# Performance work log

Hardware: AMD Instinct MI355X
Metric: run time of the kernel (lower is better)

## Reference

```python
import jax, jax.numpy as jnp
import numpy as np

DIM = 4096
N_HEADS = 32
N_KV_HEADS = 8
HEAD_DIM = DIM // N_HEADS
N_REP = N_HEADS // N_KV_HEADS
SEQ_LEN = 2048
ROPE_THETA = 10000.0


def rope_cos_sin(head_dim, seq_len, theta):
    freqs = 1.0 / (theta ** (jnp.arange(0, head_dim, 2, dtype=jnp.float32) / head_dim))  # [hd/2]
    t = jnp.arange(seq_len, dtype=jnp.float32)
    angles = jnp.outer(t, freqs)  # [S, hd/2]
    return jnp.cos(angles), jnp.sin(angles)


def apply_rope(x, cos, sin):
    # x: [B, S, H, hd]; complex rotation on interleaved (even, odd) pairs
    xr = x[..., 0::2].astype(jnp.float32)
    xi = x[..., 1::2].astype(jnp.float32)
    c = cos[None, :, None, :]
    s = sin[None, :, None, :]
    out_r = xr * c - xi * s
    out_i = xr * s + xi * c
    out = jnp.stack([out_r, out_i], axis=-1).reshape(x.shape)
    return out.astype(x.dtype)


def setup_inputs() -> dict:
    key = jax.random.key(0)
    ks = jax.random.split(key, 5)
    x = jax.random.normal(ks[0], (1, SEQ_LEN, DIM), dtype=jnp.float32)
    wq = jax.random.normal(ks[1], (DIM, DIM), dtype=jnp.float32) * (DIM ** -0.5)
    wk = jax.random.normal(ks[2], (N_KV_HEADS * HEAD_DIM, DIM), dtype=jnp.float32) * (DIM ** -0.5)
    wv = jax.random.normal(ks[3], (N_KV_HEADS * HEAD_DIM, DIM), dtype=jnp.float32) * (DIM ** -0.5)
    wo = jax.random.normal(ks[4], (DIM, DIM), dtype=jnp.float32) * (DIM ** -0.5)
    return {"x": x, "start_pos": 0, "wq": wq, "wk": wk, "wv": wv, "wo": wo}


def reference(x, start_pos, wq, wk, wv, wo):
    bsz, seq_len, _ = x.shape
    # projections (torch Linear: y = x @ W.T)
    xq = (x @ wq.T).reshape(bsz, seq_len, N_HEADS, HEAD_DIM)
    xk = (x @ wk.T).reshape(bsz, seq_len, N_KV_HEADS, HEAD_DIM)
    xv = (x @ wv.T).reshape(bsz, seq_len, N_KV_HEADS, HEAD_DIM)

    cos, sin = rope_cos_sin(HEAD_DIM, seq_len, ROPE_THETA)
    xq = apply_rope(xq, cos, sin)
    xk = apply_rope(xk, cos, sin)

    # repeat_kv (GQA): [B, S, Hkv, hd] -> [B, S, Hkv*n_rep, hd]
    keys = jnp.repeat(xk, N_REP, axis=2)
    values = jnp.repeat(xv, N_REP, axis=2)

    # [B, H, S, hd]
    q = xq.transpose(0, 2, 1, 3)
    k = keys.transpose(0, 2, 1, 3)
    v = values.transpose(0, 2, 1, 3)

    scale = 1.0 / jnp.sqrt(jnp.asarray(HEAD_DIM, dtype=jnp.float32))
    scores = jnp.einsum('bhqd,bhkd->bhqk', q, k) * scale  # [B, H, S, S]
    causal = jnp.tril(jnp.ones((seq_len, seq_len), dtype=bool))
    scores = jnp.where(causal[None, None], scores, -jnp.inf)
    attn = jax.nn.softmax(scores.astype(jnp.float32), axis=-1).astype(q.dtype)
    out = jnp.einsum('bhqk,bhkd->bhqd', attn, v)  # [B, H, S, hd]
    out = out.transpose(0, 2, 1, 3).reshape(bsz, seq_len, -1)
    return out @ wo.T
```

## Files before the change

kernel.cpp:

```cpp
#include <hip/hip_runtime.h>

#define DIM 4096
#define KVDIM 1024
#define KVSTRIDE 2048
#define SEQ 2048
#define HEADS 32
#define HD 128

typedef __attribute__((ext_vector_type(8))) short bf16x8;
typedef __attribute__((ext_vector_type(4))) float f32x4;

__device__ inline unsigned short f2bf(float f) {
    union { float f; unsigned int u; } v; v.f = f;
    unsigned int r = v.u + 0x7fffu + ((v.u >> 16) & 1u);
    return (unsigned short)(r >> 16);
}
__device__ inline float bf2f(unsigned short h) {
    union { unsigned int u; float f; } v; v.u = ((unsigned int)h) << 16;
    return v.f;
}

__device__ inline void gld16(const void* g, void* l) {
    __builtin_amdgcn_global_load_lds(
        (const __attribute__((address_space(1))) void*)g,
        (__attribute__((address_space(3))) void*)l, 16, 0, 0);
}

__global__ void convert_f32_bf16(const float* __restrict__ in,
                                 unsigned short* __restrict__ out, int n) {
    int i = (blockIdx.x * blockDim.x + threadIdx.x) * 8;
    if (i >= n) return;
    const float4* p = (const float4*)(in + i);
    float4 a = p[0], b = p[1];
    bf16x8 o;
    o[0] = (short)f2bf(a.x); o[1] = (short)f2bf(a.y);
    o[2] = (short)f2bf(a.z); o[3] = (short)f2bf(a.w);
    o[4] = (short)f2bf(b.x); o[5] = (short)f2bf(b.y);
    o[6] = (short)f2bf(b.z); o[7] = (short)f2bf(b.w);
    *(bf16x8*)(out + i) = o;
}

__global__ void rope_table(float* __restrict__ cs, float* __restrict__ sn) {
    int i = blockIdx.x * blockDim.x + threadIdx.x;
    if (i >= SEQ * 64) return;
    int m = i >> 6, f = i & 63;
    float freq = expf(-(float)f * (9.210340371976184f / 64.0f));
    float ang = (float)m * freq;
    float s, c;
    sincosf(ang, &s, &c);
    cs[i] = c; sn[i] = s;
}

__global__ void rope_apply(unsigned short* __restrict__ q, int lppr, int stride, float scale,
                           const float* __restrict__ cs, const float* __restrict__ sn) {
    int i = blockIdx.x * blockDim.x + threadIdx.x;
    int m = i >> lppr;
    int p = i & ((1 << lppr) - 1);
    if (m >= SEQ) return;
    int f = p & 63;
    int col = ((p >> 6) << 7) + (f << 1);
    size_t idx = (size_t)m * stride + col;
    unsigned int u = *(const unsigned int*)&q[idx];
    float xr = bf2f((unsigned short)(u & 0xffffu));
    float xi = bf2f((unsigned short)(u >> 16));
    float c = cs[(m << 6) + f], s = sn[(m << 6) + f];
    float orr = (xr * c - xi * s) * scale;
    float oi  = (xr * s + xi * c) * scale;
    unsigned int w = ((unsigned int)f2bf(oi) << 16) | (unsigned int)f2bf(orr);
    *(unsigned int*)&q[idx] = w;
}

template <bool OUT_BF16>
__global__ __launch_bounds__(256)
void gemm_bt(const unsigned short* __restrict__ A,
             const unsigned short* __restrict__ W,
             void* __restrict__ Cout, int M, int N, int K) {
    __shared__ __align__(16) unsigned short As[128 * 64];
    __shared__ __align__(16) unsigned short Ws[128 * 64];

    int nwg = gridDim.x * gridDim.y;
    int wg = blockIdx.y * gridDim.x + blockIdx.x;
    int cpx = nwg >> 3;
    wg = (wg & 7) * cpx + (wg >> 3);
    int bx = wg % gridDim.x, by = wg / gridDim.x;
    int brow = by * 128, bcol = bx * 128;

    int tid = threadIdx.x, lane = tid & 63, wid = tid >> 6;
    int wr = wid >> 1, wc = wid & 1, l15 = lane & 15, lq = lane >> 4;

    f32x4 acc[4][4] = {};

    for (int bk = 0; bk < K; bk += 64) {
        #pragma unroll
        for (int it = 0; it < 4; ++it) {
            int slot = it * 256 + wid * 64 + lane;
            int r = slot >> 3, g = slot & 7;
            gld16(&A[(size_t)(brow + r) * K + bk + ((g ^ (r & 7)) << 3)],
                  &As[(it * 256 + wid * 64) * 8]);
        }
        #pragma unroll
        for (int it = 0; it < 4; ++it) {
            int slot = it * 256 + wid * 64 + lane;
            int r = slot >> 3, g = slot & 7;
            gld16(&W[(size_t)(bcol + r) * K + bk + ((g ^ (r & 7)) << 3)],
                  &Ws[(it * 256 + wid * 64) * 8]);
        }
        __syncthreads();

        #pragma unroll
        for (int kk = 0; kk < 64; kk += 32) {
            int gb = (kk >> 3) + lq;
            bf16x8 af[4], bfr[4];
            #pragma unroll
            for (int m = 0; m < 4; ++m) {
                int r = wr * 64 + m * 16 + l15;
                af[m] = *(const bf16x8*)&As[r * 64 + ((gb ^ (r & 7)) << 3)];
            }
            #pragma unroll
            for (int n = 0; n < 4; ++n) {
                int r = wc * 64 + n * 16 + l15;
                bfr[n] = *(const bf16x8*)&Ws[r * 64 + ((gb ^ (r & 7)) << 3)];
            }
            #pragma unroll
            for (int m = 0; m < 4; ++m)
                #pragma unroll
                for (int n = 0; n < 4; ++n)
                    acc[m][n] = __builtin_amdgcn_mfma_f32_16x16x32_bf16(
                        af[m], bfr[n], acc[m][n], 0, 0, 0);
        }
        __syncthreads();
    }

    #pragma unroll
    for (int m = 0; m < 4; ++m) {
        #pragma unroll
        for (int n = 0; n < 4; ++n) {
            int row0 = brow + wr * 64 + m * 16 + lq * 4;
            int col = bcol + wc * 64 + n * 16 + l15;
            #pragma unroll
            for (int r = 0; r < 4; ++r) {
                if (OUT_BF16)
                    ((unsigned short*)Cout)[(size_t)(row0 + r) * N + col] = f2bf(acc[m][n][r]);
                else
                    ((float*)Cout)[(size_t)(row0 + r) * N + col] = acc[m][n][r];
            }
        }
    }
}

__global__ __launch_bounds__(256)
void attn_kernel(const unsigned short* __restrict__ Q,
                 const unsigned short* __restrict__ KV,
                 unsigned short* __restrict__ O) {
    __shared__ __align__(16) unsigned short ks[64 * 128];
    __shared__ __align__(16) unsigned short vt[128][72];
    __shared__ __align__(16) unsigned short pl[4][32][72];

    int h = blockIdx.x;
    int yy = (gridDim.y - 1) - blockIdx.y;
    int q0 = yy * 128;
    int kvh = h >> 2;
    int tid = threadIdx.x, lane = tid & 63, wid = tid >> 6;
    int l15 = lane & 15, lq = lane >> 4;
    int qr0 = q0 + wid * 32;

    bf16x8 qf[2][4];
    #pragma unroll
    for (int rf = 0; rf < 2; ++rf)
        #pragma unroll
        for (int k4 = 0; k4 < 4; ++k4)
            qf[rf][k4] = *(const bf16x8*)&Q[(size_t)(qr0 + rf * 16 + l15) * DIM + h * HD + k4 * 32 + lq * 8];

    f32x4 o_acc[2][8] = {};
    float m_run[2][4], l_run[2][4];
    #pragma unroll
    for (int rf = 0; rf < 2; ++rf)
        #pragma unroll
        for (int r = 0; r < 4; ++r) { m_run[rf][r] = -1e30f; l_run[rf][r] = 0.0f; }

    int ntiles = (q0 + 128) >> 6;
    for (int t64 = 0; t64 < ntiles; ++t64) {
        int kv0 = t64 * 64;
        #pragma unroll
        for (int it = 0; it < 4; ++it) {
            int slot = it * 256 + wid * 64 + lane;
            int r = slot >> 4, g = slot & 15;
            gld16(&KV[(size_t)(kv0 + r) * KVSTRIDE + kvh * HD + ((g ^ (r & 7)) << 3)],
                  &ks[(it * 256 + wid * 64) * 8]);
        }
        #pragma unroll
        for (int it = 0; it < 4; ++it) {
            int flat = it * 256 + tid;
            int k = flat >> 4, d0 = (flat & 15) << 3;
            bf16x8 v = *(const bf16x8*)&KV[(size_t)(kv0 + k) * KVSTRIDE + KVDIM + kvh * HD + d0];
            int swz = flat & 7;
            int cbase = (((k >> 3) ^ swz) << 3) | (k & 7);
            #pragma unroll
            for (int j = 0; j < 8; ++j)
                vt[d0 + j][cbase] = (unsigned short)v[j];
        }
        __syncthreads();

        if (kv0 <= qr0 + 31) {
            f32x4 s[2][4] = {};
            #pragma unroll
            for (int k4 = 0; k4 < 4; ++k4)
                #pragma unroll
                for (int c = 0; c < 4; ++c) {
                    int r = c * 16 + l15;
                    bf16x8 kf = *(const bf16x8*)&ks[r * 128 + ((((k4 << 2) + lq) ^ (r & 7)) << 3)];
                    s[0][c] = __builtin_amdgcn_mfma_f32_16x16x32_bf16(qf[0][k4], kf, s[0][c], 0, 0, 0);
                    s[1][c] = __builtin_amdgcn_mfma_f32_16x16x32_bf16(qf[1][k4], kf, s[1][c], 0, 0, 0);
                }

            #pragma unroll
            for (int rf = 0; rf < 2; ++rf) {
                int qrf = qr0 + rf * 16;
                if (kv0 + 63 > qrf) {
                    #pragma unroll
                    for (int c = 0; c < 4; ++c) {
                        int colg = kv0 + c * 16 + l15;
                        #pragma unroll
                        for (int r = 0; r < 4; ++r) {
                            int rowg = qrf + lq * 4 + r;
                            if (colg > rowg) s[rf][c][r] = -1e30f;
                        }
                    }
                }
                float mx[4];
                bool need = false;
                #pragma unroll
                for (int r = 0; r < 4; ++r) {
                    float e = fmaxf(fmaxf(s[rf][0][r], s[rf][1][r]),
                                    fmaxf(s[rf][2][r], s[rf][3][r]));
                    e = fmaxf(e, __shfl_xor(e, 1));
                    e = fmaxf(e, __shfl_xor(e, 2));
                    e = fmaxf(e, __shfl_xor(e, 4));
                    e = fmaxf(e, __shfl_xor(e, 8));
                    mx[r] = e;
                    need = need || (e > m_run[rf][r] + 8.0f);
                }
                if (__any((int)need)) {
                    #pragma unroll
                    for (int r = 0; r < 4; ++r) {
                        float mn = fmaxf(m_run[rf][r], mx[r]);
                        float al = exp2f(m_run[rf][r] - mn);
                        m_run[rf][r] = mn;
                        l_run[rf][r] *= al;
                        #pragma unroll
                        for (int t = 0; t < 8; ++t) o_acc[rf][t][r] *= al;
                    }
                }
                #pragma unroll
                for (int c = 0; c < 4; ++c)
                    #pragma unroll
                    for (int r = 0; r < 4; ++r) {
                        float p = exp2f(s[rf][c][r] - m_run[rf][r]);
                        l_run[rf][r] += p;
                        int prow = rf * 16 + lq * 4 + r;
                        int pcol = (c * 16 + l15) ^ (((lq * 4 + r) & 7) << 3);
                        pl[wid][prow][pcol] = (unsigned short)(__float_as_uint(p) >> 16);
                    }
            }
            asm volatile("s_waitcnt lgkmcnt(0)" ::: "memory");

            #pragma unroll
            for (int kk2 = 0; kk2 < 2; ++kk2) {
                bf16x8 pf[2];
                #pragma unroll
                for (int rf = 0; rf < 2; ++rf)
                    pf[rf] = *(const bf16x8*)&pl[wid][rf * 16 + l15]
                                               [(((kk2 << 2) + lq) ^ (l15 & 7)) << 3];
                #pragma unroll
                for (int t = 0; t < 8; ++t) {
                    int d = t * 16 + l15;
                    bf16x8 vf = *(const bf16x8*)&vt[d][(((kk2 << 2) + lq) ^ ((d >> 3) & 7)) << 3];
                    o_acc[0][t] = __builtin_amdgcn_mfma_f32_16x16x32_bf16(pf[0], vf, o_acc[0][t], 0, 0, 0);
                    o_acc[1][t] = __builtin_amdgcn_mfma_f32_16x16x32_bf16(pf[1], vf, o_acc[1][t], 0, 0, 0);
                }
            }
        }
        __syncthreads();
    }

    #pragma unroll
    for (int rf = 0; rf < 2; ++rf) {
        float rl[4];
        #pragma unroll
        for (int r = 0; r < 4; ++r) {
            float x = l_run[rf][r];
            x += __shfl_xor(x, 1);
            x += __shfl_xor(x, 2);
            x += __shfl_xor(x, 4);
            x += __shfl_xor(x, 8);
            rl[r] = __builtin_amdgcn_rcpf(x);
        }
        #pragma unroll
        for (int t = 0; t < 8; ++t)
            #pragma unroll
            for (int r = 0; r < 4; ++r)
                O[(size_t)(qr0 + rf * 16 + lq * 4 + r) * DIM + h * HD + t * 16 + l15] =
                    f2bf(o_acc[rf][t][r] * rl[r]);
    }
}

extern "C" void kernel_launch(void* const* d_in, const int* in_sizes, int n_in,
                              void* d_out, int out_size, void* d_ws, size_t ws_size,
                              hipStream_t stream) {
    const float* x  = (const float*)d_in[0];
    const float* wq = (const float*)d_in[2];
    const float* wk = (const float*)d_in[3];
    const float* wv = (const float*)d_in[4];
    const float* wo = (const float*)d_in[5];
    float* out = (float*)d_out;

    char* ws = (char*)d_ws;
    unsigned short* xb  = (unsigned short*)(ws);
    unsigned short* qb  = (unsigned short*)(ws + 16777216);
    unsigned short* kvb = (unsigned short*)(ws + 33554432);
    unsigned short* ab  = (unsigned short*)(ws + 41943040);
    float* cs = (float*)(ws + 58720256);
    float* sn = cs + SEQ * 64;
    unsigned short* wscratch = (unsigned short*)d_out;
    unsigned short* wob = (unsigned short*)(ws);

    const float SCALE2 = 0.08838834764831845f * 1.4426950408889634f;

    convert_f32_bf16<<<SEQ * DIM / 2048, 256, 0, stream>>>(x, xb, SEQ * DIM);
    rope_table<<<SEQ * 64 / 256, 256, 0, stream>>>(cs, sn);

    convert_f32_bf16<<<DIM * DIM / 2048, 256, 0, stream>>>(wq, wscratch, DIM * DIM);
    gemm_bt<true><<<dim3(DIM / 128, SEQ / 128), 256, 0, stream>>>(xb, wscratch, qb, SEQ, DIM, DIM);

    convert_f32_bf16<<<KVDIM * DIM / 2048, 256, 0, stream>>>(wk, wscratch, KVDIM * DIM);
    convert_f32_bf16<<<KVDIM * DIM / 2048, 256, 0, stream>>>(wv, wscratch + (size_t)KVDIM * DIM, KVDIM * DIM);
    gemm_bt<true><<<dim3(KVSTRIDE / 128, SEQ / 128), 256, 0, stream>>>(xb, wscratch, kvb, SEQ, KVSTRIDE, DIM);

    rope_apply<<<SEQ * (DIM / 2) / 256, 256, 0, stream>>>(qb, 11, DIM, SCALE2, cs, sn);
    rope_apply<<<SEQ * (KVDIM / 2) / 256, 256, 0, stream>>>(kvb, 9, KVSTRIDE, 1.0f, cs, sn);

    attn_kernel<<<dim3(HEADS, SEQ / 128), 256, 0, stream>>>(qb, kvb, ab);

    convert_f32_bf16<<<DIM * DIM / 2048, 256, 0, stream>>>(wo, wob, DIM * DIM);
    gemm_bt<false><<<dim3(DIM / 128, SEQ / 128), 256, 0, stream>>>(ab, wob, out, SEQ, DIM, DIM);
}
```

Baseline: 443.7 us.

## Switch attention to 32x32 MFMA with transposed S and register-held P

Rewrites the attention inner loop to use 32x32x16 bf16 MFMAs, computing S transposed (K as A operand) so each lane owns one query row. The P matrix then stays in registers via packed bf16 conversion and a lane-swap shuffle, which removes the per-warp shared-memory P buffer and its round trip. V is transposed into LDS with 32-bit packed stores instead of 16-bit scattered ones. The cost is more shuffles for the rescale and normalisation, an unswizzled V layout with padding of 66 that may cause bank conflicts on reads, and higher register pressure from the 16-wide accumulators.

```diff
diff --git a/kernel.cpp b/kernel.cpp
--- a/kernel.cpp
+++ b/kernel.cpp
@@ -9,6 +9,8 @@
 
 typedef __attribute__((ext_vector_type(8))) short bf16x8;
 typedef __attribute__((ext_vector_type(4))) float f32x4;
+typedef __attribute__((ext_vector_type(16))) float f32x16;
+typedef __attribute__((ext_vector_type(4))) int int4v;
 
 __device__ inline unsigned short f2bf(float f) {
     union { float f; unsigned int u; } v; v.f = f;
@@ -24,6 +26,12 @@
     __builtin_amdgcn_global_load_lds(
         (const __attribute__((address_space(1))) void*)g,
         (__attribute__((address_space(3))) void*)l, 16, 0, 0);
+}
+
+__device__ inline unsigned cvtpk(float a, float b) {
+    unsigned r;
+    asm("v_cvt_pk_bf16_f32 %0, %1, %2" : "=v"(r) : "v"(a), "v"(b));
+    return r;
 }
 
 __global__ void convert_f32_bf16(const float* __restrict__ in,
@@ -153,34 +161,30 @@
                  const unsigned short* __restrict__ KV,
                  unsigned short* __restrict__ O) {
     __shared__ __align__(16) unsigned short ks[64 * 128];
-    __shared__ __align__(16) unsigned short vt[128][72];
-    __shared__ __align__(16) unsigned short pl[4][32][72];
+    __shared__ __align__(16) unsigned short vt[128][66];
 
     int h = blockIdx.x;
     int yy = (gridDim.y - 1) - blockIdx.y;
     int q0 = yy * 128;
     int kvh = h >> 2;
     int tid = threadIdx.x, lane = tid & 63, wid = tid >> 6;
-    int l15 = lane & 15, lq = lane >> 4;
-    int qr0 = q0 + wid * 32;
-
-    bf16x8 qf[2][4];
+    int l31 = lane & 31, l5 = lane >> 5;
+    int qw0 = q0 + wid * 32;
+
+    bf16x8 qf[8];
     #pragma unroll
-    for (int rf = 0; rf < 2; ++rf)
-        #pragma unroll
-        for (int k4 = 0; k4 < 4; ++k4)
-            qf[rf][k4] = *(const bf16x8*)&Q[(size_t)(qr0 + rf * 16 + l15) * DIM + h * HD + k4 * 32 + lq * 8];
-
-    f32x4 o_acc[2][8] = {};
-    float m_run[2][4], l_run[2][4];
-    #pragma unroll
-    for (int rf = 0; rf < 2; ++rf)
-        #pragma unroll
-        for (int r = 0; r < 4; ++r) { m_run[rf][r] = -1e30f; l_run[rf][r] = 0.0f; }
+    for (int k8 = 0; k8 < 8; ++k8)
+        qf[k8] = *(const bf16x8*)&Q[(size_t)(qw0 + l31) * DIM + h * HD + k8 * 16 + l5 * 8];
+
+    f32x16 o_acc[4] = {};
+    float m_run = -1e30f, l_run = 0.0f;
+
+    int k4 = tid >> 4;
+    int d0 = (tid & 15) * 8;
 
     int ntiles = (q0 + 128) >> 6;
-    for (int t64 = 0; t64 < ntiles; ++t64) {
-        int kv0 = t64 * 64;
+    for (int t = 0; t < ntiles; ++t) {
+        int kv0 = t * 64;
         #pragma unroll
         for (int it = 0; it < 4; ++it) {
             int slot = it * 256 + wid * 64 + lane;
@@ -188,119 +192,110 @@
             gld16(&KV[(size_t)(kv0 + r) * KVSTRIDE + kvh * HD + ((g ^ (r & 7)) << 3)],
                   &ks[(it * 256 + wid * 64) * 8]);
         }
-        #pragma unroll
-        for (int it = 0; it < 4; ++it) {
-            int flat = it * 256 + tid;
-            int k = flat >> 4, d0 = (flat & 15) << 3;
-            bf16x8 v = *(const bf16x8*)&KV[(size_t)(kv0 + k) * KVSTRIDE + KVDIM + kvh * HD + d0];
-            int swz = flat & 7;
-            int cbase = (((k >> 3) ^ swz) << 3) | (k & 7);
-            #pragma unroll
-            for (int j = 0; j < 8; ++j)
-                vt[d0 + j][cbase] = (unsigned short)v[j];
+        {
+            bf16x8 v0 = *(const bf16x8*)&KV[(size_t)(kv0 + k4 * 4 + 0) * KVSTRIDE + KVDIM + kvh * HD + d0];
+            bf16x8 v1 = *(const bf16x8*)&KV[(size_t)(kv0 + k4 * 4 + 1) * KVSTRIDE + KVDIM + kvh * HD + d0];
+            bf16x8 v2 = *(const bf16x8*)&KV[(size_t)(kv0 + k4 * 4 + 2) * KVSTRIDE + KVDIM + kvh * HD + d0];
+            bf16x8 v3 = *(const bf16x8*)&KV[(size_t)(kv0 + k4 * 4 + 3) * KVSTRIDE + KVDIM + kvh * HD + d0];
+            #pragma unroll
+            for (int j = 0; j < 8; ++j) {
+                unsigned lo = ((unsigned)(unsigned short)v1[j] << 16) | (unsigned)(unsigned short)v0[j];
+                unsigned hi = ((unsigned)(unsigned short)v3[j] << 16) | (unsigned)(unsigned short)v2[j];
+                *(unsigned*)&vt[d0 + j][k4 * 4]     = lo;
+                *(unsigned*)&vt[d0 + j][k4 * 4 + 2] = hi;
+            }
         }
         __syncthreads();
 
-        if (kv0 <= qr0 + 31) {
-            f32x4 s[2][4] = {};
-            #pragma unroll
-            for (int k4 = 0; k4 < 4; ++k4)
-                #pragma unroll
-                for (int c = 0; c < 4; ++c) {
-                    int r = c * 16 + l15;
-                    bf16x8 kf = *(const bf16x8*)&ks[r * 128 + ((((k4 << 2) + lq) ^ (r & 7)) << 3)];
-                    s[0][c] = __builtin_amdgcn_mfma_f32_16x16x32_bf16(qf[0][k4], kf, s[0][c], 0, 0, 0);
-                    s[1][c] = __builtin_amdgcn_mfma_f32_16x16x32_bf16(qf[1][k4], kf, s[1][c], 0, 0, 0);
-                }
-
-            #pragma unroll
-            for (int rf = 0; rf < 2; ++rf) {
-                int qrf = qr0 + rf * 16;
-                if (kv0 + 63 > qrf) {
+        if (kv0 <= qw0 + 31) {
+            #pragma unroll
+            for (int sub = 0; sub < 2; ++sub) {
+                int kvs = kv0 + sub * 32;
+                if (kvs > qw0 + 31) continue;
+                f32x16 s = {};
+                #pragma unroll
+                for (int k8 = 0; k8 < 8; ++k8) {
+                    int r = sub * 32 + l31;
+                    bf16x8 kf = *(const bf16x8*)&ks[r * 128 + (((k8 * 2 + l5) ^ (r & 7)) << 3)];
+                    s = __builtin_amdgcn_mfma_f32_32x32x16_bf16(kf, qf[k8], s, 0, 0, 0);
+                }
+                if (kvs + 31 > qw0) {
                     #pragma unroll
-                    for (int c = 0; c < 4; ++c) {
-                        int colg = kv0 + c * 16 + l15;
+                    for (int r = 0; r < 16; ++r) {
+                        int kv = kvs + (r & 3) + ((r >> 2) << 3) + l5 * 4;
+                        if (kv > qw0 + l31) s[r] = -1e30f;
+                    }
+                }
+                float mx = s[0];
+                #pragma unroll
+                for (int r = 1; r < 16; ++r) mx = fmaxf(mx, s[r]);
+                mx = fmaxf(mx, __shfl_xor(mx, 32));
+                bool need = mx > m_run + 8.0f;
+                if (__any((int)need)) {
+                    float mn = fmaxf(m_run, mx);
+                    float al = exp2f(m_run - mn);
+                    m_run = mn;
+                    l_run *= al;
+                    #pragma unroll
+                    for (int r = 0; r < 16; ++r) {
+                        int qlr = (r & 3) + ((r >> 2) << 3) + l5 * 4;
+                        float alO = __shfl(al, qlr, 32);
                         #pragma unroll
-                        for (int r = 0; r < 4; ++r) {
-                            int rowg = qrf + lq * 4 + r;
-                            if (colg > rowg) s[rf][c][r] = -1e30f;
-                        }
+                        for (int t32 = 0; t32 < 4; ++t32) o_acc[t32][r] *= alO;
                     }
                 }
-                float mx[4];
-                bool need = false;
-                #pragma unroll
-                for (int r = 0; r < 4; ++r) {
-                    float e = fmaxf(fmaxf(s[rf][0][r], s[rf][1][r]),
-                                    fmaxf(s[rf][2][r], s[rf][3][r]));
-                    e = fmaxf(e, __shfl_xor(e, 1));
-                    e = fmaxf(e, __shfl_xor(e, 2));
-                    e = fmaxf(e, __shfl_xor(e, 4));
-                    e = fmaxf(e, __shfl_xor(e, 8));
-                    mx[r] = e;
-                    need = need || (e > m_run[rf][r] + 8.0f);
-                }
-                if (__any((int)need)) {
+                #pragma unroll
+                for (int r = 0; r < 16; ++r) {
+                    float p = exp2f(s[r] - m_run);
+                    l_run += p;
+                    s[r] = p;
+                }
+                bf16x8 pa[2];
+                #pragma unroll
+                for (int kk1 = 0; kk1 < 2; ++kk1) {
+                    unsigned u0 = cvtpk(s[kk1 * 8 + 0], s[kk1 * 8 + 1]);
+                    unsigned u1 = cvtpk(s[kk1 * 8 + 2], s[kk1 * 8 + 3]);
+                    unsigned u2 = cvtpk(s[kk1 * 8 + 4], s[kk1 * 8 + 5]);
+                    unsigned u3 = cvtpk(s[kk1 * 8 + 6], s[kk1 * 8 + 7]);
+                    unsigned t0 = (unsigned)__shfl_xor((int)(l5 ? u0 : u2), 32);
+                    unsigned t1 = (unsigned)__shfl_xor((int)(l5 ? u1 : u3), 32);
+                    int4v w;
+                    w.x = (int)(l5 ? t0 : u0);
+                    w.y = (int)(l5 ? t1 : u1);
+                    w.z = (int)(l5 ? u2 : t0);
+                    w.w = (int)(l5 ? u3 : t1);
+                    pa[kk1] = __builtin_bit_cast(bf16x8, w);
+                }
+                #pragma unroll
+                for (int t32 = 0; t32 < 4; ++t32) {
                     #pragma unroll
-                    for (int r = 0; r < 4; ++r) {
-                        float mn = fmaxf(m_run[rf][r], mx[r]);
-                        float al = exp2f(m_run[rf][r] - mn);
-                        m_run[rf][r] = mn;
-                        l_run[rf][r] *= al;
-                        #pragma unroll
-                        for (int t = 0; t < 8; ++t) o_acc[rf][t][r] *= al;
+                    for (int kk1 = 0; kk1 < 2; ++kk1) {
+                        const unsigned short* vrow =
+                            &vt[t32 * 32 + l31][sub * 32 + kk1 * 16 + l5 * 8];
+                        int4v w;
+                        w.x = *(const int*)&vrow[0];
+                        w.y = *(const int*)&vrow[2];
+                        w.z = *(const int*)&vrow[4];
+                        w.w = *(const int*)&vrow[6];
+                        o_acc[t32] = __builtin_amdgcn_mfma_f32_32x32x16_bf16(
+                            pa[kk1], __builtin_bit_cast(bf16x8, w), o_acc[t32], 0, 0, 0);
                     }
-                }
-                #pragma unroll
-                for (int c = 0; c < 4; ++c)
-                    #pragma unroll
-                    for (int r = 0; r < 4; ++r) {
-                        float p = exp2f(s[rf][c][r] - m_run[rf][r]);
-                        l_run[rf][r] += p;
-                        int prow = rf * 16 + lq * 4 + r;
-                        int pcol = (c * 16 + l15) ^ (((lq * 4 + r) & 7) << 3);
-                        pl[wid][prow][pcol] = (unsigned short)(__float_as_uint(p) >> 16);
-                    }
-            }
-            asm volatile("s_waitcnt lgkmcnt(0)" ::: "memory");
-
-            #pragma unroll
-            for (int kk2 = 0; kk2 < 2; ++kk2) {
-                bf16x8 pf[2];
-                #pragma unroll
-                for (int rf = 0; rf < 2; ++rf)
-                    pf[rf] = *(const bf16x8*)&pl[wid][rf * 16 + l15]
-                                               [(((kk2 << 2) + lq) ^ (l15 & 7)) << 3];
-                #pragma unroll
-                for (int t = 0; t < 8; ++t) {
-                    int d = t * 16 + l15;
-                    bf16x8 vf = *(const bf16x8*)&vt[d][(((kk2 << 2) + lq) ^ ((d >> 3) & 7)) << 3];
-                    o_acc[0][t] = __builtin_amdgcn_mfma_f32_16x16x32_bf16(pf[0], vf, o_acc[0][t], 0, 0, 0);
-                    o_acc[1][t] = __builtin_amdgcn_mfma_f32_16x16x32_bf16(pf[1], vf, o_acc[1][t], 0, 0, 0);
                 }
             }
         }
         __syncthreads();
     }
 
+    float l_tot = l_run + __shfl_xor(l_run, 32);
+    float rinv = __builtin_amdgcn_rcpf(l_tot);
     #pragma unroll
-    for (int rf = 0; rf < 2; ++rf) {
-        float rl[4];
-        #pragma unroll
-        for (int r = 0; r < 4; ++r) {
-            float x = l_run[rf][r];
-            x += __shfl_xor(x, 1);
-            x += __shfl_xor(x, 2);
-            x += __shfl_xor(x, 4);
-            x += __shfl_xor(x, 8);
-            rl[r] = __builtin_amdgcn_rcpf(x);
-        }
-        #pragma unroll
-        for (int t = 0; t < 8; ++t)
-            #pragma unroll
-            for (int r = 0; r < 4; ++r)
-                O[(size_t)(qr0 + rf * 16 + lq * 4 + r) * DIM + h * HD + t * 16 + l15] =
-                    f2bf(o_acc[rf][t][r] * rl[r]);
+    for (int r = 0; r < 16; ++r) {
+        int qlr = (r & 3) + ((r >> 2) << 3) + l5 * 4;
+        float rl = __shfl(rinv, qlr, 32);
+        #pragma unroll
+        for (int t32 = 0; t32 < 4; ++t32)
+            O[(size_t)(qw0 + qlr) * DIM + h * HD + t32 * 32 + l31] =
+                f2bf(o_acc[t32][r] * rl);
     }
 }
 
```

Result: faster. 397.9 us (-10.3%).
